# Kernel optimization log

Measured on AMD Instinct MI355X. Metric: run time of the kernel, lower is better.

The kernel has to match this reference:

```python
import jax, jax.numpy as jnp
import numpy as np

NF4 = jnp.array([-1.0, -0.6961928009986877, -0.5250730514526367, -0.39491748809814453,
                 -0.28444138169288635, -0.18477343022823334, -0.09105003625154495, 0.0,
                 0.07958029955625534, 0.16093020141124725, 0.24611230850219726,
                 0.33791524171829224, 0.44070982933044434, 0.5626170039176941,
                 0.7229568362236023, 1.0], dtype=jnp.float32)

OUT, IN = 8192, 8192
BLOCK = 64
NUMEL = OUT * IN


def setup_inputs() -> dict:
    key = jax.random.key(0)
    k1, k2, k3, k4 = jax.random.split(key, 4)
    x = jax.random.normal(k1, (64, IN), dtype=jnp.float32)
    packed = jax.random.randint(k2, (NUMEL // 2,), 0, 256, dtype=jnp.int32)
    absmax = jax.random.uniform(k3, (NUMEL // BLOCK,), dtype=jnp.float32)
    bias = jax.random.normal(k4, (OUT,), dtype=jnp.float32)
    return {"x": x, "packed": packed, "absmax": absmax, "bias": bias}


def nf4_dequantize(packed, absmax):
    # packed holds two 4-bit codes per byte: low nibble first, then high nibble
    low = packed & 15
    high = (packed >> 4) & 15
    q = jnp.stack([low, high], axis=1).reshape(-1)          # [numel]
    normalized = NF4[q]                                      # LUT dequant
    groups = normalized.reshape(-1, BLOCK)                   # [numel/block, block]
    w = (groups * absmax[:, None]).reshape(-1)[:NUMEL]
    return w.reshape(OUT, IN)


def reference(x, packed, absmax, bias):
    w = nf4_dequantize(packed, absmax)                       # [out, in]
    return jnp.dot(x, w.T) + bias                            # F.linear
```

## Files before the change

kernel.cpp:

```cpp
#include <hip/hip_runtime.h>
#include <hip/hip_bf16.h>

#define OUT_N 8192
#define IN_K  8192
#define M_ROWS 64

typedef __attribute__((ext_vector_type(8))) short  bf16x8;
typedef __attribute__((ext_vector_type(4))) float  f32x4;
typedef __attribute__((ext_vector_type(4))) int    int4v;

__device__ const float NF4_TAB[16] = {
  -1.0f, -0.6961928009986877f, -0.5250730514526367f, -0.39491748809814453f,
  -0.28444138169288635f, -0.18477343022823334f, -0.09105003625154495f, 0.0f,
  0.07958029955625534f, 0.16093020141124725f, 0.24611230850219726f,
  0.33791524171829224f, 0.44070982933044434f, 0.5626170039176941f,
  0.7229568362236023f, 1.0f };

static __device__ __forceinline__ unsigned short f2bf(float f) {
  union { __hip_bfloat16 h; unsigned short s; } u;
  u.h = __float2bfloat16(f);
  return u.s;
}

static __device__ __forceinline__ void gload_lds16(const void* g, void* s) {
  __builtin_amdgcn_global_load_lds((const __attribute__((address_space(1))) void*)g,
                                   (__attribute__((address_space(3))) void*)s,
                                   16, 0, 0);
}

__global__ __launch_bounds__(256) void qlin_prep(const float* __restrict__ x,
                                                 unsigned short* __restrict__ xf) {
  int t = blockIdx.x * 256 + threadIdx.x;
  int lane = t & 63, mt = (t >> 6) & 3, ks = t >> 8;
  int ri = lane & 15, kbb = lane >> 4;
  const float* src = x + (size_t)(mt * 16 + ri) * IN_K + ks * 32 + kbb * 8;
  f32x4 a = *(const f32x4*)src;
  f32x4 c = *(const f32x4*)(src + 4);
  bf16x8 o;
  o[0] = (short)f2bf(a[0]); o[1] = (short)f2bf(a[1]);
  o[2] = (short)f2bf(a[2]); o[3] = (short)f2bf(a[3]);
  o[4] = (short)f2bf(c[0]); o[5] = (short)f2bf(c[1]);
  o[6] = (short)f2bf(c[2]); o[7] = (short)f2bf(c[3]);
  ((bf16x8*)xf)[t] = o;
}

static __device__ __forceinline__ bf16x8 deq(const unsigned int* lut, unsigned b) {
  int4v bw;
  bw[0] = (int)lut[b & 255];
  bw[1] = (int)lut[(b >> 8) & 255];
  bw[2] = (int)lut[(b >> 16) & 255];
  bw[3] = (int)lut[b >> 24];
  union { int4v i; bf16x8 h; } c; c.i = bw;
  return c.h;
}

union SMem {
  struct {
    unsigned int lut[256];
    bf16x8 ast[2][4][128];
  } s;
  unsigned short tlb[64][72];
};

#define STAGE(BUF, PH) {                                                      \
    const char* _s = xfb + (((size_t)(PH) * 4 + w) * 4096) + l * 16;          \
    gload_lds16(_s,        &ast[BUF][w][0]);                                  \
    gload_lds16(_s + 1024, &ast[BUF][w][64]); }

#define CSTEP_BODY(S, PKV)                                                    \
    int _pks = KS + (S) + 4; if (_pks > NITm1) _pks = NITm1;                  \
    const char* _gp = xfb + (size_t)(KS + (S)) * 4096 + l * 16;               \
    bf16x8 A2 = *(const bf16x8*)(_gp + 2048);                                 \
    bf16x8 A3 = *(const bf16x8*)(_gp + 3072);                                 \
    int4v _npk = *(const int4v*)(pcoal + (size_t)_pks * 64);                  \
    bf16x8 A0 = ast[cur][S][l];                                               \
    bf16x8 A1 = ast[cur][S][64 + l];                                          \
    unsigned _pkd = (unsigned)PKV[0] | ((unsigned)PKV[1] << 8)                \
                  | ((unsigned)PKV[2] << 16) | ((unsigned)PKV[3] << 24);      \
    unsigned _bp = (unsigned)__builtin_amdgcn_ds_bpermute(bpidx, (int)_pkd);  \
    bf16x8 b = deq(lut, _bp);

#define CSTEP_EVEN(S, PKV) {                                                  \
    CSTEP_BODY(S, PKV)                                                        \
    sb0 = __builtin_amdgcn_mfma_f32_16x16x32_bf16(A0, b, zro, 0, 0, 0);       \
    sb1 = __builtin_amdgcn_mfma_f32_16x16x32_bf16(A1, b, zro, 0, 0, 0);       \
    sb2 = __builtin_amdgcn_mfma_f32_16x16x32_bf16(A2, b, zro, 0, 0, 0);       \
    sb3 = __builtin_amdgcn_mfma_f32_16x16x32_bf16(A3, b, zro, 0, 0, 0);       \
    PKV = _npk; }

#define CSTEP_ODD(S, PKV, AM) {                                               \
    CSTEP_BODY(S, PKV)                                                        \
    sb0 = __builtin_amdgcn_mfma_f32_16x16x32_bf16(A0, b, sb0, 0, 0, 0);       \
    sb1 = __builtin_amdgcn_mfma_f32_16x16x32_bf16(A1, b, sb1, 0, 0, 0);       \
    sb2 = __builtin_amdgcn_mfma_f32_16x16x32_bf16(A2, b, sb2, 0, 0, 0);       \
    sb3 = __builtin_amdgcn_mfma_f32_16x16x32_bf16(A3, b, sb3, 0, 0, 0);       \
    mn0 += sb0 * (AM); mn1 += sb1 * (AM);                                     \
    mn2 += sb2 * (AM); mn3 += sb3 * (AM);                                     \
    PKV = _npk; }

template<int NC>
__global__ __launch_bounds__(256, 4) void qlin_main(
    const int*   __restrict__ packed,
    const float* __restrict__ absmax,
    const unsigned short* __restrict__ xf,
    unsigned short* __restrict__ parts) {
  constexpr int KCn   = IN_K / NC;
  constexpr int NIT   = KCn / 32;
  constexpr int NITm1 = NIT - 1;
  constexpr int NPH   = NIT / 4;
  constexpr int AMX   = NIT / 2 - 1;
  constexpr int LOG   = (NC == 16) ? 4 : 3;

  __shared__ SMem sm;
  auto& lutm = sm.s.lut;
  auto& ast  = sm.s.ast;
  {
    int t = threadIdx.x;
    unsigned lo = f2bf(NF4_TAB[t & 15]);
    unsigned hi = f2bf(NF4_TAB[(t >> 4) & 15]);
    lutm[t] = lo | (hi << 16);
  }
  __syncthreads();
  const unsigned int* lut = &lutm[0];

  const int l     = threadIdx.x & 63;
  const int w     = threadIdx.x >> 6;
  const int ntile = (int)blockIdx.x >> LOG;
  const int chunk = (int)blockIdx.x & (NC - 1);
  const int colg0 = ntile * 64 + w * 16;
  const int col   = colg0 + (l & 15);
  const int kb    = l >> 4;
  const int kc0   = chunk * KCn;
  const int ksg0  = kc0 >> 5;

  const char* pcoal = (const char*)packed
                    + ((size_t)(colg0 + (l >> 2)) * (IN_K / 2) + kc0 / 2) * 4
                    + (l & 3) * 16;
  const int bpidx = (((l & 15) << 2) | (l >> 4)) << 2;

  const char* xfb = (const char*)xf + (size_t)ksg0 * 4096;
  const float* aptr = absmax + (size_t)col * 128 + (kc0 >> 6);

  const f32x4 zro = {0.f, 0.f, 0.f, 0.f};
  f32x4 mn0 = zro, mn1 = zro, mn2 = zro, mn3 = zro;
  f32x4 sb0, sb1, sb2, sb3;
  int4v pk0, pk1, pk2, pk3;

  float amE = aptr[0], amO = aptr[1];
  STAGE(0, 0);
  __builtin_amdgcn_sched_barrier(0);
  pk0 = *(const int4v*)(pcoal);
  pk1 = *(const int4v*)(pcoal + 64);
  pk2 = *(const int4v*)(pcoal + 128);
  pk3 = *(const int4v*)(pcoal + 192);
  asm volatile("s_waitcnt vmcnt(4)" ::: "memory");
  __builtin_amdgcn_s_barrier();

  for (int ph = 0; ph < NPH; ++ph) {
    const int KS  = ph * 4;
    const int cur = ph & 1;

    int ia = 2 * ph + 2; if (ia > AMX) ia = AMX;
    int ib = 2 * ph + 3; if (ib > AMX) ib = AMX;
    float pmE = aptr[ia], pmO = aptr[ib];
    if (ph + 1 < NPH) STAGE(cur ^ 1, ph + 1);
    __builtin_amdgcn_sched_barrier(0);

    CSTEP_EVEN(0, pk0)
    CSTEP_ODD (1, pk1, amE)
    CSTEP_EVEN(2, pk2)
    CSTEP_ODD (3, pk3, amO)

    amE = pmE; amO = pmO;
    asm volatile("s_waitcnt vmcnt(12)" ::: "memory");
    asm volatile("s_waitcnt lgkmcnt(0)" ::: "memory");
    __builtin_amdgcn_s_barrier();
  }

  {
    const int c  = w * 16 + (l & 15);
    const int r0 = kb * 4;
    sm.tlb[0  + r0 + 0][c] = f2bf(mn0[0]);
    sm.tlb[0  + r0 + 1][c] = f2bf(mn0[1]);
    sm.tlb[0  + r0 + 2][c] = f2bf(mn0[2]);
    sm.tlb[0  + r0 + 3][c] = f2bf(mn0[3]);
    sm.tlb[16 + r0 + 0][c] = f2bf(mn1[0]);
    sm.tlb[16 + r0 + 1][c] = f2bf(mn1[1]);
    sm.tlb[16 + r0 + 2][c] = f2bf(mn1[2]);
    sm.tlb[16 + r0 + 3][c] = f2bf(mn1[3]);
    sm.tlb[32 + r0 + 0][c] = f2bf(mn2[0]);
    sm.tlb[32 + r0 + 1][c] = f2bf(mn2[1]);
    sm.tlb[32 + r0 + 2][c] = f2bf(mn2[2]);
    sm.tlb[32 + r0 + 3][c] = f2bf(mn2[3]);
    sm.tlb[48 + r0 + 0][c] = f2bf(mn3[0]);
    sm.tlb[48 + r0 + 1][c] = f2bf(mn3[1]);
    sm.tlb[48 + r0 + 2][c] = f2bf(mn3[2]);
    sm.tlb[48 + r0 + 3][c] = f2bf(mn3[3]);
    __syncthreads();
    unsigned short* po = parts + ((size_t)chunk * 128 + ntile) * 4096;
    const int t   = threadIdx.x;
    const int rr  = t >> 3;
    const int oct = (t & 7) * 8;
    #pragma unroll
    for (int p = 0; p < 2; ++p) {
      const int row = p * 32 + rr;
      bf16x8 v = *(const bf16x8*)&sm.tlb[row][oct];
      *(bf16x8*)(po + (size_t)row * 64 + oct) = v;
    }
  }
}

template<int NC>
__global__ __launch_bounds__(256) void qlin_reduce(
    const unsigned short* __restrict__ parts,
    const float* __restrict__ bias,
    float*       __restrict__ out) {
  int e = blockIdx.x * 256 + threadIdx.x;
  if (e >= M_ROWS * OUT_N / 8) return;
  const int tile = e >> 9;
  const int rem  = e & 511;
  const int row  = rem >> 3;
  const int oct  = rem & 7;
  const size_t base = ((size_t)tile * 64 + row) * 64 + oct * 8;
  constexpr size_t CS = (size_t)128 * 64 * 64;
  float s[8] = {0,0,0,0,0,0,0,0};
  #pragma unroll
  for (int c = 0; c < NC; ++c) {
    bf16x8 v = *(const bf16x8*)(parts + c * CS + base);
    #pragma unroll
    for (int j = 0; j < 8; ++j)
      s[j] += __uint_as_float(((unsigned)(unsigned short)v[j]) << 16);
  }
  const int colb = tile * 64 + oct * 8;
  const f32x4* bp = (const f32x4*)(bias + colb);
  f32x4 b0 = bp[0], b1 = bp[1];
  f32x4 o0, o1;
  o0[0] = s[0] + b0[0]; o0[1] = s[1] + b0[1];
  o0[2] = s[2] + b0[2]; o0[3] = s[3] + b0[3];
  o1[0] = s[4] + b1[0]; o1[1] = s[5] + b1[1];
  o1[2] = s[6] + b1[2]; o1[3] = s[7] + b1[3];
  float* op = out + (size_t)row * OUT_N + colb;
  *(f32x4*)op = o0;
  *(f32x4*)(op + 4) = o1;
}

extern "C" void kernel_launch(void* const* d_in, const int* in_sizes, int n_in,
                              void* d_out, int out_size, void* d_ws, size_t ws_size,
                              hipStream_t stream) {
  const float* x      = (const float*)d_in[0];
  const int*   packed = (const int*)d_in[1];
  const float* absmax = (const float*)d_in[2];
  const float* bias   = (const float*)d_in[3];
  float* out = (float*)d_out;

  unsigned short* xf    = (unsigned short*)d_ws;
  unsigned short* parts = (unsigned short*)((char*)d_ws + (1 << 20));

  qlin_prep<<<(M_ROWS * IN_K / 8 + 255) / 256, 256, 0, stream>>>(x, xf);

  const size_t chunk_bytes = (size_t)128 * 64 * 64 * sizeof(unsigned short);
  const size_t need16 = (size_t)(1 << 20) + 16 * chunk_bytes;
  if (ws_size >= need16) {
    qlin_main<16><<<128 * 16, 256, 0, stream>>>(packed, absmax, xf, parts);
    qlin_reduce<16><<<(M_ROWS * OUT_N / 8 + 255) / 256, 256, 0, stream>>>(parts, bias, out);
  } else {
    qlin_main<8><<<128 * 8, 256, 0, stream>>>(packed, absmax, xf, parts);
    qlin_reduce<8><<<(M_ROWS * OUT_N / 8 + 255) / 256, 256, 0, stream>>>(parts, bias, out);
  }
}
```

Baseline: 42.80 us.

## Widen block tile to 128 columns and fold absmax scaling into dequant

Each block now covers 128 output columns, with each wave handling two 16-column groups. The four A-fragments are staged fully into LDS and reused across both groups, where before two of them were read directly from global memory each step. The absmax scale is applied per element during dequantization before the bf16 conversion. This drops the separate scaled accumulate of the MFMA results and lets the MFMAs accumulate straight into eight accumulators. In exchange it uses more registers (occupancy hint lowered to 2 waves), launches half as many blocks, and adds extra bf16 rounding of scaled weights plus more VALU work per element.

```diff
diff --git a/kernel.cpp b/kernel.cpp
--- a/kernel.cpp
+++ b/kernel.cpp
@@ -7,6 +7,7 @@
 
 typedef __attribute__((ext_vector_type(8))) short  bf16x8;
 typedef __attribute__((ext_vector_type(4))) float  f32x4;
+typedef __attribute__((ext_vector_type(2))) float  f32x2;
 typedef __attribute__((ext_vector_type(4))) int    int4v;
 
 __device__ const float NF4_TAB[16] = {
@@ -44,62 +45,67 @@
   ((bf16x8*)xf)[t] = o;
 }
 
-static __device__ __forceinline__ bf16x8 deq(const unsigned int* lut, unsigned b) {
-  int4v bw;
-  bw[0] = (int)lut[b & 255];
-  bw[1] = (int)lut[(b >> 8) & 255];
-  bw[2] = (int)lut[(b >> 16) & 255];
-  bw[3] = (int)lut[b >> 24];
-  union { int4v i; bf16x8 h; } c; c.i = bw;
-  return c.h;
+static __device__ __forceinline__ bf16x8 deqscale(const unsigned int* lut,
+                                                  unsigned b, float am) {
+  unsigned p0 = lut[b & 255];
+  unsigned p1 = lut[(b >> 8) & 255];
+  unsigned p2 = lut[(b >> 16) & 255];
+  unsigned p3 = lut[b >> 24];
+  bf16x8 r;
+  r[0] = (short)f2bf(__uint_as_float(p0 << 16) * am);
+  r[1] = (short)f2bf(__uint_as_float(p0 & 0xffff0000u) * am);
+  r[2] = (short)f2bf(__uint_as_float(p1 << 16) * am);
+  r[3] = (short)f2bf(__uint_as_float(p1 & 0xffff0000u) * am);
+  r[4] = (short)f2bf(__uint_as_float(p2 << 16) * am);
+  r[5] = (short)f2bf(__uint_as_float(p2 & 0xffff0000u) * am);
+  r[6] = (short)f2bf(__uint_as_float(p3 << 16) * am);
+  r[7] = (short)f2bf(__uint_as_float(p3 & 0xffff0000u) * am);
+  return r;
 }
 
 union SMem {
   struct {
     unsigned int lut[256];
-    bf16x8 ast[2][4][128];
+    bf16x8 ast[2][4][256];
   } s;
-  unsigned short tlb[64][72];
+  unsigned short tlb[64][136];
 };
 
 #define STAGE(BUF, PH) {                                                      \
     const char* _s = xfb + (((size_t)(PH) * 4 + w) * 4096) + l * 16;          \
     gload_lds16(_s,        &ast[BUF][w][0]);                                  \
-    gload_lds16(_s + 1024, &ast[BUF][w][64]); }
-
-#define CSTEP_BODY(S, PKV)                                                    \
-    int _pks = KS + (S) + 4; if (_pks > NITm1) _pks = NITm1;                  \
-    const char* _gp = xfb + (size_t)(KS + (S)) * 4096 + l * 16;               \
-    bf16x8 A2 = *(const bf16x8*)(_gp + 2048);                                 \
-    bf16x8 A3 = *(const bf16x8*)(_gp + 3072);                                 \
-    int4v _npk = *(const int4v*)(pcoal + (size_t)_pks * 64);                  \
+    gload_lds16(_s + 1024, &ast[BUF][w][64]);                                 \
+    gload_lds16(_s + 2048, &ast[BUF][w][128]);                                \
+    gload_lds16(_s + 3072, &ast[BUF][w][192]); }
+
+#define CSTEP(S, PKA, PKB, AMA, AMB) {                                        \
+    int _nk = KS + (S) + 2; if (_nk > NITm1) _nk = NITm1;                     \
     bf16x8 A0 = ast[cur][S][l];                                               \
     bf16x8 A1 = ast[cur][S][64 + l];                                          \
-    unsigned _pkd = (unsigned)PKV[0] | ((unsigned)PKV[1] << 8)                \
-                  | ((unsigned)PKV[2] << 16) | ((unsigned)PKV[3] << 24);      \
-    unsigned _bp = (unsigned)__builtin_amdgcn_ds_bpermute(bpidx, (int)_pkd);  \
-    bf16x8 b = deq(lut, _bp);
-
-#define CSTEP_EVEN(S, PKV) {                                                  \
-    CSTEP_BODY(S, PKV)                                                        \
-    sb0 = __builtin_amdgcn_mfma_f32_16x16x32_bf16(A0, b, zro, 0, 0, 0);       \
-    sb1 = __builtin_amdgcn_mfma_f32_16x16x32_bf16(A1, b, zro, 0, 0, 0);       \
-    sb2 = __builtin_amdgcn_mfma_f32_16x16x32_bf16(A2, b, zro, 0, 0, 0);       \
-    sb3 = __builtin_amdgcn_mfma_f32_16x16x32_bf16(A3, b, zro, 0, 0, 0);       \
-    PKV = _npk; }
-
-#define CSTEP_ODD(S, PKV, AM) {                                               \
-    CSTEP_BODY(S, PKV)                                                        \
-    sb0 = __builtin_amdgcn_mfma_f32_16x16x32_bf16(A0, b, sb0, 0, 0, 0);       \
-    sb1 = __builtin_amdgcn_mfma_f32_16x16x32_bf16(A1, b, sb1, 0, 0, 0);       \
-    sb2 = __builtin_amdgcn_mfma_f32_16x16x32_bf16(A2, b, sb2, 0, 0, 0);       \
-    sb3 = __builtin_amdgcn_mfma_f32_16x16x32_bf16(A3, b, sb3, 0, 0, 0);       \
-    mn0 += sb0 * (AM); mn1 += sb1 * (AM);                                     \
-    mn2 += sb2 * (AM); mn3 += sb3 * (AM);                                     \
-    PKV = _npk; }
+    bf16x8 A2 = ast[cur][S][128 + l];                                         \
+    bf16x8 A3 = ast[cur][S][192 + l];                                         \
+    int4v _na = *(const int4v*)(pcoalA + (size_t)_nk * 64);                   \
+    int4v _nb = *(const int4v*)(pcoalB + (size_t)_nk * 64);                   \
+    unsigned _pa = (unsigned)PKA[0] | ((unsigned)PKA[1] << 8)                 \
+                 | ((unsigned)PKA[2] << 16) | ((unsigned)PKA[3] << 24);       \
+    unsigned _pb = (unsigned)PKB[0] | ((unsigned)PKB[1] << 8)                 \
+                 | ((unsigned)PKB[2] << 16) | ((unsigned)PKB[3] << 24);       \
+    unsigned _ba = (unsigned)__builtin_amdgcn_ds_bpermute(bpidx, (int)_pa);   \
+    unsigned _bb = (unsigned)__builtin_amdgcn_ds_bpermute(bpidx, (int)_pb);   \
+    bf16x8 bA = deqscale(lut, _ba, AMA);                                      \
+    bf16x8 bB = deqscale(lut, _bb, AMB);                                      \
+    mn0 = __builtin_amdgcn_mfma_f32_16x16x32_bf16(A0, bA, mn0, 0, 0, 0);      \
+    mn1 = __builtin_amdgcn_mfma_f32_16x16x32_bf16(A1, bA, mn1, 0, 0, 0);      \
+    mn2 = __builtin_amdgcn_mfma_f32_16x16x32_bf16(A2, bA, mn2, 0, 0, 0);      \
+    mn3 = __builtin_amdgcn_mfma_f32_16x16x32_bf16(A3, bA, mn3, 0, 0, 0);      \
+    mn4 = __builtin_amdgcn_mfma_f32_16x16x32_bf16(A0, bB, mn4, 0, 0, 0);      \
+    mn5 = __builtin_amdgcn_mfma_f32_16x16x32_bf16(A1, bB, mn5, 0, 0, 0);      \
+    mn6 = __builtin_amdgcn_mfma_f32_16x16x32_bf16(A2, bB, mn6, 0, 0, 0);      \
+    mn7 = __builtin_amdgcn_mfma_f32_16x16x32_bf16(A3, bB, mn7, 0, 0, 0);      \
+    PKA = _na; PKB = _nb; }
 
 template<int NC>
-__global__ __launch_bounds__(256, 4) void qlin_main(
+__global__ __launch_bounds__(256, 2) void qlin_main(
     const int*   __restrict__ packed,
     const float* __restrict__ absmax,
     const unsigned short* __restrict__ xf,
@@ -108,51 +114,51 @@
   constexpr int NIT   = KCn / 32;
   constexpr int NITm1 = NIT - 1;
   constexpr int NPH   = NIT / 4;
-  constexpr int AMX   = NIT / 2 - 1;
   constexpr int LOG   = (NC == 16) ? 4 : 3;
 
   __shared__ SMem sm;
-  auto& lutm = sm.s.lut;
-  auto& ast  = sm.s.ast;
+  auto& ast = sm.s.ast;
   {
     int t = threadIdx.x;
     unsigned lo = f2bf(NF4_TAB[t & 15]);
     unsigned hi = f2bf(NF4_TAB[(t >> 4) & 15]);
-    lutm[t] = lo | (hi << 16);
+    sm.s.lut[t] = lo | (hi << 16);
   }
   __syncthreads();
-  const unsigned int* lut = &lutm[0];
+  const unsigned int* lut = &sm.s.lut[0];
 
   const int l     = threadIdx.x & 63;
   const int w     = threadIdx.x >> 6;
   const int ntile = (int)blockIdx.x >> LOG;
   const int chunk = (int)blockIdx.x & (NC - 1);
-  const int colg0 = ntile * 64 + w * 16;
-  const int col   = colg0 + (l & 15);
+  const int c0    = ntile * 128 + w * 32;
+  const int colA  = c0 + (l & 15);
   const int kb    = l >> 4;
   const int kc0   = chunk * KCn;
   const int ksg0  = kc0 >> 5;
 
-  const char* pcoal = (const char*)packed
-                    + ((size_t)(colg0 + (l >> 2)) * (IN_K / 2) + kc0 / 2) * 4
-                    + (l & 3) * 16;
+  const char* pcoalA = (const char*)packed
+                     + ((size_t)(c0 + (l >> 2)) * (IN_K / 2) + kc0 / 2) * 4
+                     + (l & 3) * 16;
+  const char* pcoalB = pcoalA + (size_t)16 * (IN_K / 2) * 4;
   const int bpidx = (((l & 15) << 2) | (l >> 4)) << 2;
 
   const char* xfb = (const char*)xf + (size_t)ksg0 * 4096;
-  const float* aptr = absmax + (size_t)col * 128 + (kc0 >> 6);
+  const f32x2* aptrA = (const f32x2*)(absmax + (size_t)colA * 128 + (kc0 >> 6));
+  const f32x2* aptrB = (const f32x2*)(absmax + (size_t)(colA + 16) * 128 + (kc0 >> 6));
 
   const f32x4 zro = {0.f, 0.f, 0.f, 0.f};
   f32x4 mn0 = zro, mn1 = zro, mn2 = zro, mn3 = zro;
-  f32x4 sb0, sb1, sb2, sb3;
-  int4v pk0, pk1, pk2, pk3;
-
-  float amE = aptr[0], amO = aptr[1];
+  f32x4 mn4 = zro, mn5 = zro, mn6 = zro, mn7 = zro;
+  int4v pkA0, pkA1, pkB0, pkB1;
+
+  f32x2 amA = aptrA[0], amB = aptrB[0];
   STAGE(0, 0);
   __builtin_amdgcn_sched_barrier(0);
-  pk0 = *(const int4v*)(pcoal);
-  pk1 = *(const int4v*)(pcoal + 64);
-  pk2 = *(const int4v*)(pcoal + 128);
-  pk3 = *(const int4v*)(pcoal + 192);
+  pkA0 = *(const int4v*)(pcoalA);
+  pkA1 = *(const int4v*)(pcoalA + 64);
+  pkB0 = *(const int4v*)(pcoalB);
+  pkB1 = *(const int4v*)(pcoalB + 64);
   asm volatile("s_waitcnt vmcnt(4)" ::: "memory");
   __builtin_amdgcn_s_barrier();
 
@@ -160,52 +166,67 @@
     const int KS  = ph * 4;
     const int cur = ph & 1;
 
-    int ia = 2 * ph + 2; if (ia > AMX) ia = AMX;
-    int ib = 2 * ph + 3; if (ib > AMX) ib = AMX;
-    float pmE = aptr[ia], pmO = aptr[ib];
+    int pn = ph + 1; if (pn > NPH - 1) pn = NPH - 1;
+    f32x2 pmA = aptrA[pn], pmB = aptrB[pn];
     if (ph + 1 < NPH) STAGE(cur ^ 1, ph + 1);
     __builtin_amdgcn_sched_barrier(0);
 
-    CSTEP_EVEN(0, pk0)
-    CSTEP_ODD (1, pk1, amE)
-    CSTEP_EVEN(2, pk2)
-    CSTEP_ODD (3, pk3, amO)
-
-    amE = pmE; amO = pmO;
-    asm volatile("s_waitcnt vmcnt(12)" ::: "memory");
+    CSTEP(0, pkA0, pkB0, amA[0], amB[0])
+    CSTEP(1, pkA1, pkB1, amA[0], amB[0])
+    CSTEP(2, pkA0, pkB0, amA[1], amB[1])
+    CSTEP(3, pkA1, pkB1, amA[1], amB[1])
+
+    amA = pmA; amB = pmB;
+    asm volatile("s_waitcnt vmcnt(4)" ::: "memory");
     asm volatile("s_waitcnt lgkmcnt(0)" ::: "memory");
     __builtin_amdgcn_s_barrier();
   }
 
   {
-    const int c  = w * 16 + (l & 15);
+    const int ca = w * 32 + (l & 15);
     const int r0 = kb * 4;
-    sm.tlb[0  + r0 + 0][c] = f2bf(mn0[0]);
-    sm.tlb[0  + r0 + 1][c] = f2bf(mn0[1]);
-    sm.tlb[0  + r0 + 2][c] = f2bf(mn0[2]);
-    sm.tlb[0  + r0 + 3][c] = f2bf(mn0[3]);
-    sm.tlb[16 + r0 + 0][c] = f2bf(mn1[0]);
-    sm.tlb[16 + r0 + 1][c] = f2bf(mn1[1]);
-    sm.tlb[16 + r0 + 2][c] = f2bf(mn1[2]);
-    sm.tlb[16 + r0 + 3][c] = f2bf(mn1[3]);
-    sm.tlb[32 + r0 + 0][c] = f2bf(mn2[0]);
-    sm.tlb[32 + r0 + 1][c] = f2bf(mn2[1]);
-    sm.tlb[32 + r0 + 2][c] = f2bf(mn2[2]);
-    sm.tlb[32 + r0 + 3][c] = f2bf(mn2[3]);
-    sm.tlb[48 + r0 + 0][c] = f2bf(mn3[0]);
-    sm.tlb[48 + r0 + 1][c] = f2bf(mn3[1]);
-    sm.tlb[48 + r0 + 2][c] = f2bf(mn3[2]);
-    sm.tlb[48 + r0 + 3][c] = f2bf(mn3[3]);
+    sm.tlb[0  + r0 + 0][ca] = f2bf(mn0[0]);
+    sm.tlb[0  + r0 + 1][ca] = f2bf(mn0[1]);
+    sm.tlb[0  + r0 + 2][ca] = f2bf(mn0[2]);
+    sm.tlb[0  + r0 + 3][ca] = f2bf(mn0[3]);
+    sm.tlb[16 + r0 + 0][ca] = f2bf(mn1[0]);
+    sm.tlb[16 + r0 + 1][ca] = f2bf(mn1[1]);
+    sm.tlb[16 + r0 + 2][ca] = f2bf(mn1[2]);
+    sm.tlb[16 + r0 + 3][ca] = f2bf(mn1[3]);
+    sm.tlb[32 + r0 + 0][ca] = f2bf(mn2[0]);
+    sm.tlb[32 + r0 + 1][ca] = f2bf(mn2[1]);
+    sm.tlb[32 + r0 + 2][ca] = f2bf(mn2[2]);
+    sm.tlb[32 + r0 + 3][ca] = f2bf(mn2[3]);
+    sm.tlb[48 + r0 + 0][ca] = f2bf(mn3[0]);
+    sm.tlb[48 + r0 + 1][ca] = f2bf(mn3[1]);
+    sm.tlb[48 + r0 + 2][ca] = f2bf(mn3[2]);
+    sm.tlb[48 + r0 + 3][ca] = f2bf(mn3[3]);
+    const int cb = ca + 16;
+    sm.tlb[0  + r0 + 0][cb] = f2bf(mn4[0]);
+    sm.tlb[0  + r0 + 1][cb] = f2bf(mn4[1]);
+    sm.tlb[0  + r0 + 2][cb] = f2bf(mn4[2]);
+    sm.tlb[0  + r0 + 3][cb] = f2bf(mn4[3]);
+    sm.tlb[16 + r0 + 0][cb] = f2bf(mn5[0]);
+    sm.tlb[16 + r0 + 1][cb] = f2bf(mn5[1]);
+    sm.tlb[16 + r0 + 2][cb] = f2bf(mn5[2]);
+    sm.tlb[16 + r0 + 3][cb] = f2bf(mn5[3]);
+    sm.tlb[32 + r0 + 0][cb] = f2bf(mn6[0]);
+    sm.tlb[32 + r0 + 1][cb] = f2bf(mn6[1]);
+    sm.tlb[32 + r0 + 2][cb] = f2bf(mn6[2]);
+    sm.tlb[32 + r0 + 3][cb] = f2bf(mn6[3]);
+    sm.tlb[48 + r0 + 0][cb] = f2bf(mn7[0]);
+    sm.tlb[48 + r0 + 1][cb] = f2bf(mn7[1]);
+    sm.tlb[48 + r0 + 2][cb] = f2bf(mn7[2]);
+    sm.tlb[48 + r0 + 3][cb] = f2bf(mn7[3]);
     __syncthreads();
-    unsigned short* po = parts + ((size_t)chunk * 128 + ntile) * 4096;
-    const int t   = threadIdx.x;
-    const int rr  = t >> 3;
-    const int oct = (t & 7) * 8;
+    unsigned short* po = parts + ((size_t)chunk * 64 + ntile) * 8192;
     #pragma unroll
-    for (int p = 0; p < 2; ++p) {
-      const int row = p * 32 + rr;
+    for (int p = 0; p < 4; ++p) {
+      const int item = p * 256 + (int)threadIdx.x;
+      const int row  = item >> 4;
+      const int oct  = (item & 15) * 8;
       bf16x8 v = *(const bf16x8*)&sm.tlb[row][oct];
-      *(bf16x8*)(po + (size_t)row * 64 + oct) = v;
+      *(bf16x8*)(po + (size_t)row * 128 + oct) = v;
     }
   }
 }
@@ -217,12 +238,12 @@
     float*       __restrict__ out) {
   int e = blockIdx.x * 256 + threadIdx.x;
   if (e >= M_ROWS * OUT_N / 8) return;
-  const int tile = e >> 9;
-  const int rem  = e & 511;
-  const int row  = rem >> 3;
-  const int oct  = rem & 7;
-  const size_t base = ((size_t)tile * 64 + row) * 64 + oct * 8;
-  constexpr size_t CS = (size_t)128 * 64 * 64;
+  const int tile = e >> 10;
+  const int rem  = e & 1023;
+  const int row  = rem >> 4;
+  const int oct  = rem & 15;
+  const size_t base = ((size_t)tile * 64 + row) * 128 + oct * 8;
+  constexpr size_t CS = (size_t)64 * 64 * 128;
   float s[8] = {0,0,0,0,0,0,0,0};
   #pragma unroll
   for (int c = 0; c < NC; ++c) {
@@ -231,7 +252,7 @@
     for (int j = 0; j < 8; ++j)
       s[j] += __uint_as_float(((unsigned)(unsigned short)v[j]) << 16);
   }
-  const int colb = tile * 64 + oct * 8;
+  const int colb = tile * 128 + oct * 8;
   const f32x4* bp = (const f32x4*)(bias + colb);
   f32x4 b0 = bp[0], b1 = bp[1];
   f32x4 o0, o1;
@@ -258,13 +279,13 @@
 
   qlin_prep<<<(M_ROWS * IN_K / 8 + 255) / 256, 256, 0, stream>>>(x, xf);
 
-  const size_t chunk_bytes = (size_t)128 * 64 * 64 * sizeof(unsigned short);
+  const size_t chunk_bytes = (size_t)64 * 64 * 128 * sizeof(unsigned short);
   const size_t need16 = (size_t)(1 << 20) + 16 * chunk_bytes;
   if (ws_size >= need16) {
-    qlin_main<16><<<128 * 16, 256, 0, stream>>>(packed, absmax, xf, parts);
+    qlin_main<16><<<64 * 16, 256, 0, stream>>>(packed, absmax, xf, parts);
     qlin_reduce<16><<<(M_ROWS * OUT_N / 8 + 255) / 256, 256, 0, stream>>>(parts, bias, out);
   } else {
-    qlin_main<8><<<128 * 8, 256, 0, stream>>>(packed, absmax, xf, parts);
+    qlin_main<8><<<64 * 8, 256, 0, stream>>>(packed, absmax, xf, parts);
     qlin_reduce<8><<<(M_ROWS * OUT_N / 8 + 255) / 256, 256, 0, stream>>>(parts, bias, out);
   }
 }
```

Result: no change. 43.36 us (+1.3%).
